# Performance work log

Measured on AMD Instinct MI355X. Metric: run time of the kernel, lower is better.

Reference implementation:

```python
import jax, jax.numpy as jnp
import numpy as np

B, C, H, W = 128, 1024, 16, 12
CI = 512              # inter_channels = in_channels // 2
EPS = 1e-4            # module's self.eps for std normalization
BN_EPS = 1e-5         # torch BatchNorm2d default eps (eval mode, running stats)


def setup_inputs() -> dict:
    key = jax.random.key(0)
    ks = jax.random.split(key, 8)
    s_in = 1.0 / np.sqrt(C)
    s_192 = 1.0 / np.sqrt(192)
    s_64 = 1.0 / np.sqrt(64)
    return {
        "x": jax.random.normal(ks[0], (B, C, H, W), jnp.float32),
        "theta_w": jax.random.normal(ks[1], (CI, C), jnp.float32) * s_in,
        "theta_b": jax.random.normal(ks[2], (CI,), jnp.float32) * s_in,
        "phi_w": jax.random.normal(ks[3], (CI, C), jnp.float32) * s_in,
        "phi_b": jax.random.normal(ks[4], (CI,), jnp.float32) * s_in,
        "m1_w": jax.random.normal(ks[5], (64, H * W), jnp.float32) * s_192,
        "m1_b": jax.random.normal(ks[6], (64,), jnp.float32) * s_192,
        "bn_g": jnp.ones((64,), jnp.float32),
        "bn_b": jnp.zeros((64,), jnp.float32),
        "bn_m": jnp.zeros((64,), jnp.float32),
        "bn_v": jnp.ones((64,), jnp.float32),
        "m2_w": jax.random.normal(ks[7], (1, 64), jnp.float32) * s_64,
        "m2_b": jnp.zeros((1,), jnp.float32),
    }


def _conv1x1(x, w, b):
    # x: (B, Cin, H, W), w: (Cout, Cin) -> (B, Cout, H, W)
    return jnp.einsum("bchw,oc->bohw", x, w) + b[None, :, None, None]


def reference(x, theta_w, theta_b, phi_w, phi_b, m1_w, m1_b,
              bn_g, bn_b, bn_m, bn_v, m2_w, m2_b):
    b, c, h, w = x.shape
    hw = h * w

    # theta/phi 1x1 conv projections -> (B, CI, HW)
    theta = _conv1x1(x, theta_w, theta_b).reshape(b, CI, hw)
    phi = _conv1x1(x, phi_w, phi_b).reshape(b, CI, hw)

    # theta_x: (B, HW, CI), z-score over channel axis (torch.std unbiased, ddof=1)
    theta_x = jnp.transpose(theta, (0, 2, 1))
    theta_x = theta_x - jnp.mean(theta_x, axis=2, keepdims=True)
    theta_x = theta_x / (jnp.std(theta_x, axis=2, keepdims=True, ddof=1) + EPS)

    # phi_x: (B, CI, HW), z-score over channel axis (dim 1)
    phi_x = phi - jnp.mean(phi, axis=1, keepdims=True)
    phi_x = phi_x / (jnp.std(phi_x, axis=1, keepdims=True, ddof=1) + EPS)

    # correlation: (B, HW, HW), divided by phi_x.size(1) == CI
    f = jnp.einsum("bnc,bcm->bnm", theta_x, phi_x) / CI

    # transpose then view as (B, HW, H, W) image of correlation maps
    mc = jnp.transpose(f, (0, 2, 1)).reshape(b, hw, h, w)

    # spatial_mask_summary: conv1x1(192->64) -> BN (eval) -> ReLU -> conv1x1(64->1)
    t = _conv1x1(mc, m1_w, m1_b)
    t = (t - bn_m[None, :, None, None]) * (
        bn_g[None, :, None, None] / jnp.sqrt(bn_v + BN_EPS)[None, :, None, None]
    ) + bn_b[None, :, None, None]
    t = jax.nn.relu(t)
    mask = jax.nn.sigmoid(_conv1x1(t, m2_w, m2_b))  # (B, 1, H, W)

    # sigmoid-gated residual
    return x + mask * x
```

## Files before the change

kernel.cpp:

```cpp
#include <hip/hip_runtime.h>

#define B_N 128
#define C_N 1024
#define HW_N 192
#define CI_N 512
#define MROWS (B_N * HW_N)

typedef short bf16x8 __attribute__((ext_vector_type(8)));
typedef float f32x4 __attribute__((ext_vector_type(4)));
typedef unsigned short us4 __attribute__((ext_vector_type(4)));
typedef unsigned short us8 __attribute__((ext_vector_type(8)));

__device__ __forceinline__ unsigned short f2bf(float f){
    unsigned int u = __builtin_bit_cast(unsigned int, f);
    u += 0x7fffu + ((u >> 16) & 1u);
    return (unsigned short)(u >> 16);
}
__device__ __forceinline__ float bf2f(unsigned short h){
    unsigned int u = ((unsigned int)h) << 16;
    return __builtin_bit_cast(float, u);
}
__device__ __forceinline__ void gload_lds16(const void* g, void* l){
    __builtin_amdgcn_global_load_lds(
        (const __attribute__((address_space(1))) unsigned int*)g,
        (__attribute__((address_space(3))) unsigned int*)l, 16, 0, 0);
}

__global__ __launch_bounds__(256) void k_prep_x(const float* __restrict__ x,
                                                unsigned short* __restrict__ xbT){
    __shared__ float tile[64][37];
    int b  = blockIdx.z;
    int c0 = blockIdx.y * 64;
    int n0 = blockIdx.x * 32;
    int t  = threadIdx.x;
    const float* xp = x + (size_t)b * C_N * HW_N;
    int cr = t >> 3;
    int nw = (t & 7) * 4;
    #pragma unroll
    for (int i = 0; i < 2; ++i){
        float4 v = *(const float4*)(xp + (size_t)(c0 + cr + 32 * i) * HW_N + n0 + nw);
        tile[cr + 32 * i][nw + 0] = v.x;
        tile[cr + 32 * i][nw + 1] = v.y;
        tile[cr + 32 * i][nw + 2] = v.z;
        tile[cr + 32 * i][nw + 3] = v.w;
    }
    __syncthreads();
    int nl = t >> 3;
    int j  = t & 7;
    us8 pk;
    #pragma unroll
    for (int e = 0; e < 8; ++e)
        pk[e] = f2bf(tile[j * 8 + e][nl]);
    *(us8*)(xbT + (size_t)(b * HW_N + n0 + nl) * C_N + c0 + j * 8) = pk;
}

__global__ __launch_bounds__(256) void k_prep_w(const float* __restrict__ tw, const float* __restrict__ tb,
                                                const float* __restrict__ pw, const float* __restrict__ pb,
                                                const float* __restrict__ m1w,
                                                unsigned short* __restrict__ Wc, float* __restrict__ bias,
                                                unsigned short* __restrict__ w1b){
    int i = blockIdx.x * 256 + threadIdx.x;
    int o = i >> 10, c = i & 1023;
    float v = (o < 512) ? tw[(size_t)o * 1024 + c] : pw[(size_t)(o - 512) * 1024 + c];
    Wc[i] = f2bf(v);
    if (i < 1024) bias[i] = (i < 512) ? tb[i] : pb[i - 512];
    if (i < 64 * HW_N) w1b[i] = f2bf(m1w[i]);
}

__global__ __launch_bounds__(256, 3) void k_gemm1(const unsigned short* __restrict__ Wc,
                                               const float* __restrict__ bias,
                                               const unsigned short* __restrict__ xbT,
                                               unsigned short* __restrict__ TPt,
                                               float2* __restrict__ part){
    __shared__ __align__(16) unsigned short lW[128 * 64];
    __shared__ __align__(16) unsigned short lX[128 * 64];
    int bid  = blockIdx.x;
    int xcd  = bid & 7;
    int slot = bid >> 3;
    int mb = xcd * 24 + (slot >> 3);
    int nb = slot & 7;
    int tid = threadIdx.x, lane = tid & 63, wave = tid >> 6;
    int wr = wave >> 1, wc = wave & 1;
    int fr = lane & 15, fg = lane >> 4;

    const unsigned short* Wg = Wc  + (size_t)(nb * 128) * C_N;
    const unsigned short* Xg = xbT + (size_t)(mb * 128) * C_N;

    int row0 = tid >> 3;
    int su   = tid & 7;
    int gsw  = (su ^ (row0 & 7)) * 8;
    const unsigned short* wsrc = Wg + (size_t)row0 * C_N + gsw;
    const unsigned short* xsrc = Xg + (size_t)row0 * C_N + gsw;

    f32x4 acc[4][4];
    f32x4 zero = {0.f, 0.f, 0.f, 0.f};
    #pragma unroll
    for (int i = 0; i < 4; ++i)
        #pragma unroll
        for (int j = 0; j < 4; ++j)
            acc[i][j] = zero;

    for (int k0 = 0; k0 < C_N; k0 += 64){
        __syncthreads();
        #pragma unroll
        for (int i = 0; i < 4; ++i){
            gload_lds16(wsrc + (size_t)(32 * i) * C_N + k0, (char*)lW + tid * 16 + i * 4096);
            gload_lds16(xsrc + (size_t)(32 * i) * C_N + k0, (char*)lX + tid * 16 + i * 4096);
        }
        __syncthreads();

        #pragma unroll
        for (int kk = 0; kk < 2; ++kk){
            bf16x8 wf[4], xf[4];
            #pragma unroll
            for (int j = 0; j < 4; ++j){
                int row = wc * 64 + j * 16 + fr;
                int un  = (kk * 4 + fg) ^ (row & 7);
                wf[j] = *(const bf16x8*)((char*)lW + row * 128 + un * 16);
            }
            #pragma unroll
            for (int i = 0; i < 4; ++i){
                int row = wr * 64 + i * 16 + fr;
                int un  = (kk * 4 + fg) ^ (row & 7);
                xf[i] = *(const bf16x8*)((char*)lX + row * 128 + un * 16);
            }
            #pragma unroll
            for (int i = 0; i < 4; ++i)
                #pragma unroll
                for (int j = 0; j < 4; ++j)
                    acc[i][j] = __builtin_amdgcn_mfma_f32_16x16x32_bf16(wf[j], xf[i], acc[i][j], 0, 0, 0);
        }
    }

    float s[4] = {0.f,0.f,0.f,0.f}, q[4] = {0.f,0.f,0.f,0.f};
    #pragma unroll
    for (int i = 0; i < 4; ++i){
        int n = mb * 128 + wr * 64 + i * 16 + fr;
        #pragma unroll
        for (int j = 0; j < 4; ++j){
            int o0 = nb * 128 + wc * 64 + j * 16 + fg * 4;
            float4 b4 = *(const float4*)(bias + o0);
            float v0 = acc[i][j][0] + b4.x;
            float v1 = acc[i][j][1] + b4.y;
            float v2 = acc[i][j][2] + b4.z;
            float v3 = acc[i][j][3] + b4.w;
            s[i] += v0 + v1 + v2 + v3;
            q[i] += v0*v0 + v1*v1 + v2*v2 + v3*v3;
            us4 pk;
            pk[0] = f2bf(v0); pk[1] = f2bf(v1); pk[2] = f2bf(v2); pk[3] = f2bf(v3);
            *(us4*)(TPt + (size_t)n * 1024 + o0) = pk;
        }
    }
    #pragma unroll
    for (int i = 0; i < 4; ++i){
        s[i] += __shfl_xor(s[i], 16); s[i] += __shfl_xor(s[i], 32);
        q[i] += __shfl_xor(q[i], 16); q[i] += __shfl_xor(q[i], 32);
    }
    if (lane < 16){
        int chunk = nb * 2 + wc;
        #pragma unroll
        for (int i = 0; i < 4; ++i){
            int n = mb * 128 + wr * 64 + i * 16 + fr;
            part[(size_t)n * 16 + chunk] = make_float2(s[i], q[i]);
        }
    }
}

__global__ __launch_bounds__(256) void k_stats(const float2* __restrict__ part,
                                               float2* __restrict__ stats){
    int idx = blockIdx.x * 256 + threadIdx.x;
    int n = idx >> 1, h = idx & 1;
    const float2* p = part + (size_t)n * 16 + h * 8;
    float S = 0.f, Q = 0.f;
    #pragma unroll
    for (int k = 0; k < 8; ++k){ float2 v = p[k]; S += v.x; Q += v.y; }
    float mean = S * (1.f / 512.f);
    float var  = (Q - 512.f * mean * mean) * (1.f / 511.f);
    float inv  = 1.f / (sqrtf(fmaxf(var, 0.f)) + 1e-4f);
    stats[idx] = make_float2(mean, inv);
}

__global__ __launch_bounds__(256) void k_gemm2m(const unsigned short* __restrict__ TPt,
        const float2* __restrict__ stats,
        const unsigned short* __restrict__ w1b, const float* __restrict__ m1b,
        const float* __restrict__ bng, const float* __restrict__ bnb,
        const float* __restrict__ bnm, const float* __restrict__ bnv,
        const float* __restrict__ m2w, const float* __restrict__ m2b,
        float* __restrict__ mask){
    __shared__ __align__(16) unsigned short lT[64 * 64];
    __shared__ __align__(16) unsigned short lP[192 * 64];
    __shared__ __align__(16) unsigned short lF[64 * 200];
    int tn = blockIdx.x;
    int b  = blockIdx.y;
    int tid = threadIdx.x, lane = tid & 63, wave = tid >> 6;
    int wr = wave >> 1, wc = wave & 1;
    int fr = lane & 15, fg = lane >> 4;

    int rbase = tid >> 3;
    int su    = tid & 7;
    const unsigned short* src[8];
    float2 st[8];
    unsigned short* dst[8];
    #pragma unroll
    for (int i = 0; i < 8; ++i){
        int srow = rbase + 32 * i;
        int swz  = (su ^ (srow & 7)) * 16;
        if (i < 2){
            int gn = b * HW_N + tn * 64 + srow;
            src[i] = TPt + (size_t)gn * 1024 + su * 8;
            st[i]  = stats[(size_t)gn * 2 + 0];
            dst[i] = (unsigned short*)((char*)lT + srow * 128 + swz);
        } else {
            int prow = srow - 64;
            int gm = b * HW_N + prow;
            src[i] = TPt + (size_t)gm * 1024 + 512 + su * 8;
            st[i]  = stats[(size_t)gm * 2 + 1];
            dst[i] = (unsigned short*)((char*)lP + prow * 128 + swz);
        }
    }

    f32x4 acc[3][2][2];
    f32x4 zero = {0.f, 0.f, 0.f, 0.f};
    #pragma unroll
    for (int t = 0; t < 3; ++t)
        #pragma unroll
        for (int i = 0; i < 2; ++i)
            #pragma unroll
            for (int j = 0; j < 2; ++j)
                acc[t][i][j] = zero;

    for (int k0 = 0; k0 < CI_N; k0 += 64){
        bf16x8 nv[8];
        #pragma unroll
        for (int i = 0; i < 8; ++i){
            bf16x8 v = *(const bf16x8*)(src[i] + k0);
            #pragma unroll
            for (int e = 0; e < 8; ++e)
                nv[i][e] = (short)f2bf((bf2f((unsigned short)v[e]) - st[i].x) * st[i].y);
        }
        __syncthreads();
        #pragma unroll
        for (int i = 0; i < 8; ++i)
            *(bf16x8*)dst[i] = nv[i];
        __syncthreads();

        #pragma unroll
        for (int kk = 0; kk < 2; ++kk){
            bf16x8 tf[2];
            #pragma unroll
            for (int i = 0; i < 2; ++i){
                int row = wr * 32 + i * 16 + fr;
                int un  = (kk * 4 + fg) ^ (row & 7);
                tf[i] = *(const bf16x8*)((char*)lT + row * 128 + un * 16);
            }
            #pragma unroll
            for (int t = 0; t < 3; ++t){
                #pragma unroll
                for (int j = 0; j < 2; ++j){
                    int row = t * 64 + wc * 32 + j * 16 + fr;
                    int un  = (kk * 4 + fg) ^ (row & 7);
                    bf16x8 pf = *(const bf16x8*)((char*)lP + row * 128 + un * 16);
                    #pragma unroll
                    for (int i = 0; i < 2; ++i)
                        acc[t][i][j] = __builtin_amdgcn_mfma_f32_16x16x32_bf16(pf, tf[i], acc[t][i][j], 0, 0, 0);
                }
            }
        }
    }

    __syncthreads();
    #pragma unroll
    for (int t = 0; t < 3; ++t)
        #pragma unroll
        for (int i = 0; i < 2; ++i){
            int n = wr * 32 + i * 16 + fr;
            #pragma unroll
            for (int j = 0; j < 2; ++j){
                int m0 = t * 64 + wc * 32 + j * 16 + fg * 4;
                us4 pk;
                #pragma unroll
                for (int r = 0; r < 4; ++r)
                    pk[r] = f2bf(acc[t][i][j][r] * (1.0f / 512.0f));
                *(us4*)((char*)lF + ((size_t)n * 200 + m0) * 2) = pk;
            }
        }
    __syncthreads();

    f32x4 macc[4];
    #pragma unroll
    for (int j = 0; j < 4; ++j) macc[j] = zero;
    #pragma unroll
    for (int kk = 0; kk < 6; ++kk){
        bf16x8 af = *(const bf16x8*)((char*)lF + ((size_t)(wave * 16 + fr) * 200 + kk * 32 + fg * 8) * 2);
        #pragma unroll
        for (int j = 0; j < 4; ++j){
            bf16x8 bfv = *(const bf16x8*)(w1b + (size_t)(j * 16 + fr) * HW_N + kk * 32 + fg * 8);
            macc[j] = __builtin_amdgcn_mfma_f32_16x16x32_bf16(af, bfv, macc[j], 0, 0, 0);
        }
    }
    float sc[4], sh[4], bb[4], w2v[4];
    #pragma unroll
    for (int j = 0; j < 4; ++j){
        int o = j * 16 + fr;
        float s = bng[o] * rsqrtf(bnv[o] + 1e-5f);
        sc[j] = s;
        sh[j] = bnb[o] - bnm[o] * s;
        bb[j] = m1b[o];
        w2v[j] = m2w[o];
    }
    float mb2 = m2b[0];
    #pragma unroll
    for (int r = 0; r < 4; ++r){
        float y = 0.f;
        #pragma unroll
        for (int j = 0; j < 4; ++j){
            float t = fmaxf((macc[j][r] + bb[j]) * sc[j] + sh[j], 0.f);
            y += t * w2v[j];
        }
        y += __shfl_xor(y, 1);
        y += __shfl_xor(y, 2);
        y += __shfl_xor(y, 4);
        y += __shfl_xor(y, 8);
        if (fr == 0)
            mask[(size_t)b * HW_N + tn * 64 + wave * 16 + fg * 4 + r] = 1.f / (1.f + __expf(-(y + mb2)));
    }
}

__global__ __launch_bounds__(256) void k_apply(const float* __restrict__ x,
                                               const float* __restrict__ mask,
                                               float* __restrict__ out){
    size_t i4 = (size_t)blockIdx.x * 256 + threadIdx.x;
    size_t e  = i4 * 4;
    float4 v = ((const float4*)x)[i4];
    size_t n = e % HW_N;
    size_t b = e / ((size_t)C_N * HW_N);
    const float* mk = mask + b * HW_N + n;
    float4 o;
    o.x = v.x * (1.f + mk[0]);
    o.y = v.y * (1.f + mk[1]);
    o.z = v.z * (1.f + mk[2]);
    o.w = v.w * (1.f + mk[3]);
    ((float4*)out)[i4] = o;
}

extern "C" void kernel_launch(void* const* d_in, const int* in_sizes, int n_in,
                              void* d_out, int out_size, void* d_ws, size_t ws_size,
                              hipStream_t stream){
    (void)in_sizes; (void)n_in; (void)out_size; (void)ws_size;
    const float* x   = (const float*)d_in[0];
    const float* tw  = (const float*)d_in[1];
    const float* tb  = (const float*)d_in[2];
    const float* pw  = (const float*)d_in[3];
    const float* pb  = (const float*)d_in[4];
    const float* m1w = (const float*)d_in[5];
    const float* m1b = (const float*)d_in[6];
    const float* bng = (const float*)d_in[7];
    const float* bnb = (const float*)d_in[8];
    const float* bnm = (const float*)d_in[9];
    const float* bnv = (const float*)d_in[10];
    const float* m2w = (const float*)d_in[11];
    const float* m2b = (const float*)d_in[12];
    float* out = (float*)d_out;

    char* ws = (char*)d_ws;
    size_t off = 0;
    unsigned short* xbT = (unsigned short*)(ws + off); off += (size_t)MROWS * C_N * 2;
    unsigned short* Wc  = (unsigned short*)(ws + off); off += (size_t)1024 * 1024 * 2;
    float* bias         = (float*)(ws + off);          off += 4096;
    unsigned short* TPt = (unsigned short*)(ws + off); off += (size_t)MROWS * 1024 * 2;
    float* mask         = (float*)(ws + off);          off += (size_t)MROWS * 4;
    unsigned short* w1b = (unsigned short*)(ws + off); off += (size_t)64 * HW_N * 2;
    off = (off + 255) & ~(size_t)255;
    float2* part        = (float2*)(ws + off);         off += (size_t)MROWS * 16 * 8;
    float2* stats       = (float2*)(ws + off);         off += (size_t)MROWS * 2 * 8;

    k_prep_x<<<dim3(6, 16, B_N), 256, 0, stream>>>(x, xbT);
    k_prep_w<<<dim3(4096), 256, 0, stream>>>(tw, tb, pw, pb, m1w, Wc, bias, w1b);
    k_gemm1<<<dim3(1536), 256, 0, stream>>>(Wc, bias, xbT, TPt, part);
    k_stats<<<dim3(MROWS * 2 / 256), 256, 0, stream>>>(part, stats);
    k_gemm2m<<<dim3(3, B_N), 256, 0, stream>>>(TPt, stats, w1b, m1b, bng, bnb, bnm, bnv, m2w, m2b, mask);
    k_apply<<<dim3(MROWS * C_N / 4 / 256), 256, 0, stream>>>(x, mask, out);
}
```

Before: 164.7 us.

## Enlarge projection GEMM tiles to 256x256 with double-buffered LDS prefetch

Rewrites the theta/phi projection GEMM so each 512-thread block computes a 256x256 output tile instead of 128x128. The next K slice is double-buffered in LDS and prefetched in chunks interleaved with MFMA phases, using explicit waitcnt, barriers and setprio. The goal is to raise operand reuse per LDS byte and to hide global-load latency behind compute. In exchange, each wave holds more accumulator registers, the block uses 128KB of LDS, and far fewer blocks are launched (384), which may hurt occupancy and tail balance.

```diff
diff --git a/kernel.cpp b/kernel.cpp
--- a/kernel.cpp
+++ b/kernel.cpp
@@ -67,24 +67,24 @@
     if (i < 64 * HW_N) w1b[i] = f2bf(m1w[i]);
 }
 
-__global__ __launch_bounds__(256, 3) void k_gemm1(const unsigned short* __restrict__ Wc,
+__global__ __launch_bounds__(512, 2) void k_gemm1(const unsigned short* __restrict__ Wc,
                                                const float* __restrict__ bias,
                                                const unsigned short* __restrict__ xbT,
                                                unsigned short* __restrict__ TPt,
                                                float2* __restrict__ part){
-    __shared__ __align__(16) unsigned short lW[128 * 64];
-    __shared__ __align__(16) unsigned short lX[128 * 64];
+    __shared__ __align__(16) unsigned short lW[2][256 * 64];
+    __shared__ __align__(16) unsigned short lX[2][256 * 64];
     int bid  = blockIdx.x;
     int xcd  = bid & 7;
     int slot = bid >> 3;
-    int mb = xcd * 24 + (slot >> 3);
-    int nb = slot & 7;
+    int mb = xcd * 12 + (slot >> 2);
+    int nb = slot & 3;
     int tid = threadIdx.x, lane = tid & 63, wave = tid >> 6;
-    int wr = wave >> 1, wc = wave & 1;
+    int wm = wave >> 2, wn = wave & 3;
     int fr = lane & 15, fg = lane >> 4;
 
-    const unsigned short* Wg = Wc  + (size_t)(nb * 128) * C_N;
-    const unsigned short* Xg = xbT + (size_t)(mb * 128) * C_N;
+    const unsigned short* Wg = Wc  + (size_t)(nb * 256) * C_N;
+    const unsigned short* Xg = xbT + (size_t)(mb * 256) * C_N;
 
     int row0 = tid >> 3;
     int su   = tid & 7;
@@ -92,53 +92,113 @@
     const unsigned short* wsrc = Wg + (size_t)row0 * C_N + gsw;
     const unsigned short* xsrc = Xg + (size_t)row0 * C_N + gsw;
 
-    f32x4 acc[4][4];
+#define STAGE_CHUNK(c, buf, kcol)                                                         \
+    do {                                                                                  \
+        const unsigned short* _b = ((c) < 2 ? wsrc : xsrc) + (size_t)(((c)&1) * 128) * C_N + (kcol); \
+        char* _d = (char*)((c) < 2 ? lW[buf] : lX[buf]) + ((c)&1) * 16384 + tid * 16;     \
+        gload_lds16(_b, _d);                                                              \
+        gload_lds16(_b + (size_t)64 * C_N, _d + 8192);                                    \
+    } while (0)
+
+    f32x4 acc[8][4];
     f32x4 zero = {0.f, 0.f, 0.f, 0.f};
     #pragma unroll
-    for (int i = 0; i < 4; ++i)
+    for (int i = 0; i < 8; ++i)
         #pragma unroll
         for (int j = 0; j < 4; ++j)
             acc[i][j] = zero;
 
-    for (int k0 = 0; k0 < C_N; k0 += 64){
-        __syncthreads();
-        #pragma unroll
-        for (int i = 0; i < 4; ++i){
-            gload_lds16(wsrc + (size_t)(32 * i) * C_N + k0, (char*)lW + tid * 16 + i * 4096);
-            gload_lds16(xsrc + (size_t)(32 * i) * C_N + k0, (char*)lX + tid * 16 + i * 4096);
-        }
-        __syncthreads();
-
-        #pragma unroll
-        for (int kk = 0; kk < 2; ++kk){
-            bf16x8 wf[4], xf[4];
-            #pragma unroll
-            for (int j = 0; j < 4; ++j){
-                int row = wc * 64 + j * 16 + fr;
-                int un  = (kk * 4 + fg) ^ (row & 7);
-                wf[j] = *(const bf16x8*)((char*)lW + row * 128 + un * 16);
-            }
-            #pragma unroll
-            for (int i = 0; i < 4; ++i){
-                int row = wr * 64 + i * 16 + fr;
-                int un  = (kk * 4 + fg) ^ (row & 7);
-                xf[i] = *(const bf16x8*)((char*)lX + row * 128 + un * 16);
-            }
-            #pragma unroll
-            for (int i = 0; i < 4; ++i)
-                #pragma unroll
-                for (int j = 0; j < 4; ++j)
-                    acc[i][j] = __builtin_amdgcn_mfma_f32_16x16x32_bf16(wf[j], xf[i], acc[i][j], 0, 0, 0);
-        }
-    }
-
-    float s[4] = {0.f,0.f,0.f,0.f}, q[4] = {0.f,0.f,0.f,0.f};
-    #pragma unroll
-    for (int i = 0; i < 4; ++i){
-        int n = mb * 128 + wr * 64 + i * 16 + fr;
+    STAGE_CHUNK(0, 0, 0);
+    STAGE_CHUNK(1, 0, 0);
+    STAGE_CHUNK(2, 0, 0);
+    STAGE_CHUNK(3, 0, 0);
+
+    for (int kt = 0; kt < 16; ++kt){
+        int cur = kt & 1, nxt = cur ^ 1;
+        int k1 = (kt + 1) * 64;
+        bool pre = (kt < 15);
+
+        if (pre){
+            STAGE_CHUNK(0, nxt, k1);
+            asm volatile("s_waitcnt vmcnt(2)" ::: "memory");
+        } else {
+            asm volatile("s_waitcnt vmcnt(0)" ::: "memory");
+        }
+        __builtin_amdgcn_sched_barrier(0);
+        __builtin_amdgcn_s_barrier();
+
+        bf16x8 wf[4][2];
         #pragma unroll
         for (int j = 0; j < 4; ++j){
-            int o0 = nb * 128 + wc * 64 + j * 16 + fg * 4;
+            int row = wn * 64 + j * 16 + fr;
+            #pragma unroll
+            for (int kk = 0; kk < 2; ++kk)
+                wf[j][kk] = *(const bf16x8*)((const char*)lW[cur] + row * 128 + (((kk * 4 + fg) ^ (row & 7)) * 16));
+        }
+        {
+            bf16x8 xf[2][2];
+            #pragma unroll
+            for (int di = 0; di < 2; ++di){
+                int row = wm * 128 + di * 16 + fr;
+                #pragma unroll
+                for (int kk = 0; kk < 2; ++kk)
+                    xf[di][kk] = *(const bf16x8*)((const char*)lX[cur] + row * 128 + (((kk * 4 + fg) ^ (row & 7)) * 16));
+            }
+            asm volatile("s_waitcnt lgkmcnt(0)" ::: "memory");
+            __builtin_amdgcn_sched_barrier(0);
+            __builtin_amdgcn_s_setprio(1);
+            #pragma unroll
+            for (int kk = 0; kk < 2; ++kk)
+                #pragma unroll
+                for (int di = 0; di < 2; ++di)
+                    #pragma unroll
+                    for (int j = 0; j < 4; ++j)
+                        acc[di][j] = __builtin_amdgcn_mfma_f32_16x16x32_bf16(wf[j][kk], xf[di][kk], acc[di][j], 0, 0, 0);
+            __builtin_amdgcn_s_setprio(0);
+        }
+        __builtin_amdgcn_s_barrier();
+
+        #pragma unroll
+        for (int p = 1; p < 4; ++p){
+            bf16x8 xf[2][2];
+            #pragma unroll
+            for (int di = 0; di < 2; ++di){
+                int row = wm * 128 + (p * 2 + di) * 16 + fr;
+                #pragma unroll
+                for (int kk = 0; kk < 2; ++kk)
+                    xf[di][kk] = *(const bf16x8*)((const char*)lX[cur] + row * 128 + (((kk * 4 + fg) ^ (row & 7)) * 16));
+            }
+            if (pre){
+                if (p == 1) STAGE_CHUNK(1, nxt, k1);
+                if (p == 2) STAGE_CHUNK(2, nxt, k1);
+                if (p == 3) STAGE_CHUNK(3, nxt, k1);
+            }
+            __builtin_amdgcn_s_barrier();
+            asm volatile("s_waitcnt lgkmcnt(0)" ::: "memory");
+            __builtin_amdgcn_sched_barrier(0);
+            __builtin_amdgcn_s_setprio(1);
+            #pragma unroll
+            for (int kk = 0; kk < 2; ++kk)
+                #pragma unroll
+                for (int di = 0; di < 2; ++di)
+                    #pragma unroll
+                    for (int j = 0; j < 4; ++j)
+                        acc[p * 2 + di][j] = __builtin_amdgcn_mfma_f32_16x16x32_bf16(wf[j][kk], xf[di][kk], acc[p * 2 + di][j], 0, 0, 0);
+            __builtin_amdgcn_s_setprio(0);
+            __builtin_amdgcn_s_barrier();
+        }
+    }
+#undef STAGE_CHUNK
+
+    float s[8], q[8];
+    #pragma unroll
+    for (int i = 0; i < 8; ++i){ s[i] = 0.f; q[i] = 0.f; }
+    #pragma unroll
+    for (int i = 0; i < 8; ++i){
+        int n = mb * 256 + wm * 128 + i * 16 + fr;
+        #pragma unroll
+        for (int j = 0; j < 4; ++j){
+            int o0 = nb * 256 + wn * 64 + j * 16 + fg * 4;
             float4 b4 = *(const float4*)(bias + o0);
             float v0 = acc[i][j][0] + b4.x;
             float v1 = acc[i][j][1] + b4.y;
@@ -152,15 +212,15 @@
         }
     }
     #pragma unroll
-    for (int i = 0; i < 4; ++i){
+    for (int i = 0; i < 8; ++i){
         s[i] += __shfl_xor(s[i], 16); s[i] += __shfl_xor(s[i], 32);
         q[i] += __shfl_xor(q[i], 16); q[i] += __shfl_xor(q[i], 32);
     }
-    if (lane < 16){
-        int chunk = nb * 2 + wc;
-        #pragma unroll
-        for (int i = 0; i < 4; ++i){
-            int n = mb * 128 + wr * 64 + i * 16 + fr;
+    if (fg == 0){
+        int chunk = nb * 4 + wn;
+        #pragma unroll
+        for (int i = 0; i < 8; ++i){
+            int n = mb * 256 + wm * 128 + i * 16 + fr;
             part[(size_t)n * 16 + chunk] = make_float2(s[i], q[i]);
         }
     }
@@ -376,7 +436,7 @@
 
     k_prep_x<<<dim3(6, 16, B_N), 256, 0, stream>>>(x, xbT);
     k_prep_w<<<dim3(4096), 256, 0, stream>>>(tw, tb, pw, pb, m1w, Wc, bias, w1b);
-    k_gemm1<<<dim3(1536), 256, 0, stream>>>(Wc, bias, xbT, TPt, part);
+    k_gemm1<<<dim3(384), 512, 0, stream>>>(Wc, bias, xbT, TPt, part);
     k_stats<<<dim3(MROWS * 2 / 256), 256, 0, stream>>>(part, stats);
     k_gemm2m<<<dim3(3, B_N), 256, 0, stream>>>(TPt, stats, w1b, m1b, bng, bnb, bnm, bnv, m2w, m2b, mask);
     k_apply<<<dim3(MROWS * C_N / 4 / 256), 256, 0, stream>>>(x, mask, out);
```

Measured after the change: 178.9 us. +8.7%, slower.
